# Optimization experiments

Measured on AMD Instinct MI355X. Metric: run time of the kernel, lower is better.

## Reference

```python
import jax, jax.numpy as jnp
import numpy as np

B, N, DN, DT = 1024, 200, 128, 128
M = DN + DN + DT  # model_dim = 384 (node + edge + time dims)


def setup_inputs() -> dict:
    key = jax.random.key(0)
    ks = jax.random.split(key, 10)
    rn = lambda k, s, sc=1.0: jax.random.normal(k, s, jnp.float32) * sc
    return {
        'src': rn(ks[0], (B, DN)),
        'src_t': rn(ks[1], (B, 1, DT)),
        'seq': rn(ks[2], (B, N, DN)),
        'seq_t': rn(ks[3], (B, N, DT)),
        'seq_e': rn(ks[4], (B, N, DN)),
        'mask': jax.random.randint(ks[5], (B, N), 0, 2).astype(bool),
        'shared_attn': rn(ks[6], (1, 2 * M), 0.05),
        'fc_w': rn(ks[7], (M, M), 0.05),
        'ln_g': jnp.ones((M,), jnp.float32),
        'ln_b': jnp.zeros((M,), jnp.float32),
        'agg_fc_w1': rn(ks[8], (2 * DN, M + DN), 0.05),
        'agg_fc_w2': rn(ks[9], (DN, 2 * DN), 0.05),
    }


def _layer_norm(x, g, b, eps=1e-5):
    mu = x.mean(-1, keepdims=True)
    var = ((x - mu) ** 2).mean(-1, keepdims=True)
    return (x - mu) * jax.lax.rsqrt(var + eps) * g + b


def reference(src, src_t, seq, seq_t, seq_e, mask, shared_attn, fc_w, ln_g, ln_b, agg_fc_w1, agg_fc_w2):
    # AttnModel.forward with 'simple' Attention (eval mode: dropout off)
    src_ext = src[:, None, :]                                   # [B,1,DN]
    q = jnp.concatenate([src_ext, jnp.zeros_like(src_ext), src_t], axis=2)  # [B,1,M]
    k = jnp.concatenate([seq, seq_e, seq_t], axis=2)            # [B,N,M]
    # F.linear(cat([q_exp, k_exp], -1), shared_attn) == q.w_q + k.w_k (fused, avoids [B,1,N,2M])
    w = shared_attn[0]
    wq, wk = w[:M], w[M:]
    scores = jnp.einsum('bqd,d->bq', q, wq)[:, :, None] + jnp.einsum('bnd,d->bn', k, wk)[:, None, :]  # [B,1,N]
    scores = jnp.where(mask[:, None, :], -1e10, scores)
    attn = jax.nn.softmax(scores, axis=2)                       # [B,1,N]
    out = jnp.einsum('bqn,bnm->bqm', attn, k)                   # [B,1,M] (v == k)
    out = out @ fc_w.T
    out = _layer_norm(out + q, ln_g, ln_b)
    out = out[:, 0, :]                                          # [B,M]
    attn_w = attn[:, 0, :]                                      # [B,N]
    x = jnp.concatenate([out, src], axis=1)                     # [B, M+DN]
    x = jax.nn.relu(x @ agg_fc_w1.T)                            # [B, 2*DN]
    out = x @ agg_fc_w2.T                                       # [B, DN]
    return out, attn_w
```

## Files before the change

kernel.cpp:

```cpp
#include <hip/hip_runtime.h>


constexpr int B_   = 1024;
constexpr int N_   = 200;
constexpr int DN_  = 128;
constexpr int DT_  = 128;
constexpr int M_   = 384;
constexpr int BDIM = 512;
constexpr int ROWS = 2;
constexpr int WPR  = 4;
constexpr int NPW  = N_ / WPR;
constexpr int PAIRS = NPW / 2;

__device__ float g_fcT[M_ * M_];
__device__ float g_w1T[(M_ + DN_) * (2 * DN_)];
__device__ float g_w2T[(2 * DN_) * DN_];

__device__ __forceinline__ float half_sum(float v) {
#pragma unroll
    for (int off = 16; off > 0; off >>= 1) v += __shfl_xor(v, off, 64);
    return v;
}
__device__ __forceinline__ float wave_sum(float v) {
#pragma unroll
    for (int off = 32; off > 0; off >>= 1) v += __shfl_xor(v, off, 64);
    return v;
}

__global__ void transpose_weights(const float* __restrict__ fc_w,
                                  const float* __restrict__ w1,
                                  const float* __restrict__ w2) {
    const int stride = gridDim.x * blockDim.x;
    for (int idx = blockIdx.x * blockDim.x + threadIdx.x; idx < M_ * M_; idx += stride) {
        const int j = idx / M_, i = idx - j * M_;
        g_fcT[idx] = fc_w[i * M_ + j];
    }
    for (int idx = blockIdx.x * blockDim.x + threadIdx.x; idx < (M_ + DN_) * (2 * DN_); idx += stride) {
        const int j = idx >> 8, i = idx & 255;
        g_w1T[idx] = w1[i * (M_ + DN_) + j];
    }
    for (int idx = blockIdx.x * blockDim.x + threadIdx.x; idx < (2 * DN_) * DN_; idx += stride) {
        const int j = idx >> 7, i = idx & 127;
        g_w2T[idx] = w2[i * (2 * DN_) + j];
    }
}

__global__ __launch_bounds__(BDIM)
void tgnn_kernel(
    const float* __restrict__ src,
    const float* __restrict__ src_t,
    const float* __restrict__ seq,
    const float* __restrict__ seq_t,
    const float* __restrict__ seq_e,
    const int*   __restrict__ mask,
    const float* __restrict__ shared_attn,
    const float* __restrict__ ln_g,
    const float* __restrict__ ln_b,
    float* __restrict__ out,
    float* __restrict__ attn_out)
{
    const int blk  = blockIdx.x;
    const int tid  = threadIdx.x;
    const int wave = tid >> 6;
    const int lane = tid & 63;
    const int row  = wave >> 2;
    const int wir  = wave & 3;
    const int b    = blk * ROWS + row;
    const int half = lane >> 5;
    const int sub  = lane & 31;
    const int c0   = 4 * sub;

    __shared__ float s_p[ROWS][N_];
    __shared__ float s_q[ROWS][M_];
    __shared__ float s_oa[8][M_];
    __shared__ float s_x[ROWS][M_];
    __shared__ float s_y[ROWS][M_ + DN_];
    __shared__ float s_h[ROWS][2 * DN_];
    __shared__ int   s_mask[ROWS][N_];
    __shared__ float s_red[ROWS][8];

    for (int idx = tid; idx < ROWS * M_; idx += BDIM) {
        const int r = idx / M_, d = idx - r * M_;
        const int bb = blk * ROWS + r;
        float v = (d < DN_) ? src[bb * DN_ + d]
                            : (d < 2 * DN_ ? 0.0f : src_t[bb * DT_ + (d - 2 * DN_)]);
        s_q[r][d] = v;
    }
    for (int idx = tid; idx < ROWS * N_; idx += BDIM) {
        const int r = idx / N_, n = idx - r * N_;
        s_mask[r][n] = mask[(blk * ROWS + r) * N_ + n];
    }

    const float* wq = shared_attn;
    const float* wk = shared_attn + M_;
    const float4 wkA = *(const float4*)&wk[c0];
    const float4 wkE = *(const float4*)&wk[DN_ + c0];
    const float4 wkT = *(const float4*)&wk[2 * DN_ + c0];
    const float4 wqA = *(const float4*)&wq[c0];
    const float4 wqT = *(const float4*)&wq[2 * DN_ + c0];

    __syncthreads();

    const float4 qa = *(const float4*)&s_q[row][c0];
    const float4 qt = *(const float4*)&s_q[row][2 * DN_ + c0];
    float qp = qa.x * wqA.x + qa.y * wqA.y + qa.z * wqA.z + qa.w * wqA.w
             + qt.x * wqT.x + qt.y * wqT.y + qt.z * wqT.z + qt.w * wqT.w;
    const float qdot = half_sum(qp);

    const int nb = wir * NPW + half;
    const float* baseA = seq   + (long)b * (N_ * DN_);
    const float* baseE = seq_e + (long)b * (N_ * DN_);
    const float* baseT = seq_t + (long)b * (N_ * DT_);
    int off = nb * DN_ + c0;
    int n   = nb;

    float4 oA = make_float4(0.f, 0.f, 0.f, 0.f);
    float4 oE = oA, oT = oA;
    float lsum = 0.f;

    int pairs = PAIRS;
    asm volatile("" : "+s"(pairs));
#pragma unroll 1
    for (int it = 0; it < pairs; ++it) {
        const float4 a = *(const float4*)(baseA + off);
        const float4 e = *(const float4*)(baseE + off);
        const float4 t = *(const float4*)(baseT + off);
        float part = a.x * wkA.x + a.y * wkA.y + a.z * wkA.z + a.w * wkA.w
                   + e.x * wkE.x + e.y * wkE.y + e.z * wkE.z + e.w * wkE.w
                   + t.x * wkT.x + t.y * wkT.y + t.z * wkT.z + t.w * wkT.w;
        part = half_sum(part);
        const float p = s_mask[row][n] ? 0.0f : __expf(part + qdot);
        if (sub == 0) s_p[row][n] = p;
        lsum += p;
        oA.x += p * a.x; oA.y += p * a.y; oA.z += p * a.z; oA.w += p * a.w;
        oE.x += p * e.x; oE.y += p * e.y; oE.z += p * e.z; oE.w += p * e.w;
        oT.x += p * t.x; oT.y += p * t.y; oT.z += p * t.z; oT.w += p * t.w;
        off += 2 * DN_;
        n   += 2;
    }

    oA.x += __shfl_xor(oA.x, 32, 64); oA.y += __shfl_xor(oA.y, 32, 64);
    oA.z += __shfl_xor(oA.z, 32, 64); oA.w += __shfl_xor(oA.w, 32, 64);
    oE.x += __shfl_xor(oE.x, 32, 64); oE.y += __shfl_xor(oE.y, 32, 64);
    oE.z += __shfl_xor(oE.z, 32, 64); oE.w += __shfl_xor(oE.w, 32, 64);
    oT.x += __shfl_xor(oT.x, 32, 64); oT.y += __shfl_xor(oT.y, 32, 64);
    oT.z += __shfl_xor(oT.z, 32, 64); oT.w += __shfl_xor(oT.w, 32, 64);
    lsum += __shfl_xor(lsum, 32, 64);
    if (lane == 0) s_red[row][wir] = lsum;
    if (half == 0) {
        *(float4*)&s_oa[wave][c0]            = oA;
        *(float4*)&s_oa[wave][DN_ + c0]      = oE;
        *(float4*)&s_oa[wave][2 * DN_ + c0]  = oT;
    }
    __syncthreads();

    for (int idx = tid; idx < ROWS * M_; idx += BDIM) {
        const int r = idx / M_, d = idx - r * M_;
        const float Z = s_red[r][0] + s_red[r][1] + s_red[r][2] + s_red[r][3];
        const float invZ = 1.0f / Z;
        s_x[r][d] = (s_oa[4 * r + 0][d] + s_oa[4 * r + 1][d] +
                     s_oa[4 * r + 2][d] + s_oa[4 * r + 3][d]) * invZ;
    }
    for (int idx = tid; idx < ROWS * N_; idx += BDIM) {
        const int r = idx / N_, nn = idx - r * N_;
        const float Z = s_red[r][0] + s_red[r][1] + s_red[r][2] + s_red[r][3];
        attn_out[(blk * ROWS + r) * N_ + nn] = s_p[r][nn] * (1.0f / Z);
    }
    __syncthreads();

    if (tid < M_) {
        float acc0 = 0.f, acc1 = 0.f;
#pragma unroll 8
        for (int j = 0; j < M_; ++j) {
            const float w = g_fcT[j * M_ + tid];
            acc0 += s_x[0][j] * w;
            acc1 += s_x[1][j] * w;
        }
        s_y[0][tid] = acc0 + s_q[0][tid];
        s_y[1][tid] = acc1 + s_q[1][tid];
    }
    __syncthreads();

    {
        float ls = 0.f, lq = 0.f;
        for (int j = 64 * wir + lane; j < M_; j += 256) {
            const float v = s_y[row][j];
            ls += v; lq += v * v;
        }
        ls = wave_sum(ls); lq = wave_sum(lq);
        if (lane == 0) { s_red[row][wir] = ls; s_red[row][4 + wir] = lq; }
    }
    __syncthreads();
    for (int idx = tid; idx < ROWS * M_; idx += BDIM) {
        const int r = idx / M_, j = idx - r * M_;
        const float mean = (s_red[r][0] + s_red[r][1] + s_red[r][2] + s_red[r][3]) * (1.0f / M_);
        const float msq  = (s_red[r][4] + s_red[r][5] + s_red[r][6] + s_red[r][7]) * (1.0f / M_);
        const float rstd = rsqrtf(msq - mean * mean + 1e-5f);
        s_y[r][j] = (s_y[r][j] - mean) * rstd * ln_g[j] + ln_b[j];
    }
    for (int idx = tid; idx < ROWS * DN_; idx += BDIM) {
        const int r = idx >> 7, d = idx & 127;
        s_y[r][M_ + d] = s_q[r][d];
    }
    __syncthreads();

    {
        const int r = tid >> 8, i = tid & 255;
        float acc = 0.f;
#pragma unroll 8
        for (int j = 0; j < M_ + DN_; ++j)
            acc += s_y[r][j] * g_w1T[j * 256 + i];
        s_h[r][i] = fmaxf(acc, 0.0f);
    }
    __syncthreads();

    if (tid < 256) {
        const int r = tid >> 7, i = tid & 127;
        float acc = 0.f;
#pragma unroll 8
        for (int j = 0; j < 2 * DN_; ++j)
            acc += s_h[r][j] * g_w2T[j * 128 + i];
        out[(blk * ROWS + r) * DN_ + i] = acc;
    }
}

extern "C" void kernel_launch(void* const* d_in, const int* in_sizes, int n_in,
                              void* d_out, int out_size, void* d_ws, size_t ws_size,
                              hipStream_t stream) {
    const float* src         = (const float*)d_in[0];
    const float* src_t       = (const float*)d_in[1];
    const float* seq         = (const float*)d_in[2];
    const float* seq_t       = (const float*)d_in[3];
    const float* seq_e       = (const float*)d_in[4];
    const int*   mask        = (const int*)  d_in[5];
    const float* shared_attn = (const float*)d_in[6];
    const float* fc_w        = (const float*)d_in[7];
    const float* ln_g        = (const float*)d_in[8];
    const float* ln_b        = (const float*)d_in[9];
    const float* w1          = (const float*)d_in[10];
    const float* w2          = (const float*)d_in[11];

    float* outp     = (float*)d_out;
    float* attn_out = (float*)d_out + B_ * DN_;

    transpose_weights<<<256, 256, 0, stream>>>(fc_w, w1, w2);
    tgnn_kernel<<<B_ / ROWS, BDIM, 0, stream>>>(src, src_t, seq, seq_t, seq_e, mask,
                                                shared_attn, ln_g, ln_b, outp, attn_out);
}
```

Measured before the change: 380.6 us.

## Double block size to 8 waves per row and split MLP reductions over K

```diff
diff --git a/kernel.cpp b/kernel.cpp
--- a/kernel.cpp
+++ b/kernel.cpp
@@ -6,11 +6,11 @@
 constexpr int DN_  = 128;
 constexpr int DT_  = 128;
 constexpr int M_   = 384;
-constexpr int BDIM = 512;
+constexpr int BDIM = 1024;
 constexpr int ROWS = 2;
-constexpr int WPR  = 4;
+constexpr int WPR  = 8;
 constexpr int NPW  = N_ / WPR;
-constexpr int PAIRS = NPW / 2;
+constexpr int ITER = (NPW + 1) / 2;
 
 __device__ float g_fcT[M_ * M_];
 __device__ float g_w1T[(M_ + DN_) * (2 * DN_)];
@@ -63,8 +63,8 @@
     const int tid  = threadIdx.x;
     const int wave = tid >> 6;
     const int lane = tid & 63;
-    const int row  = wave >> 2;
-    const int wir  = wave & 3;
+    const int row  = wave >> 3;
+    const int wir  = wave & 7;
     const int b    = blk * ROWS + row;
     const int half = lane >> 5;
     const int sub  = lane & 31;
@@ -72,12 +72,14 @@
 
     __shared__ float s_p[ROWS][N_];
     __shared__ float s_q[ROWS][M_];
-    __shared__ float s_oa[8][M_];
+    __shared__ float s_oa[16][M_];
     __shared__ float s_x[ROWS][M_];
     __shared__ float s_y[ROWS][M_ + DN_];
     __shared__ float s_h[ROWS][2 * DN_];
     __shared__ int   s_mask[ROWS][N_];
-    __shared__ float s_red[ROWS][8];
+    __shared__ float s_red[ROWS][16];
+    __shared__ float s_w1p[2][ROWS][256];
+    __shared__ float s_w2p[4][ROWS][128];
 
     for (int idx = tid; idx < ROWS * M_; idx += BDIM) {
         const int r = idx / M_, d = idx - r * M_;
@@ -107,21 +109,23 @@
              + qt.x * wqT.x + qt.y * wqT.y + qt.z * wqT.z + qt.w * wqT.w;
     const float qdot = half_sum(qp);
 
-    const int nb = wir * NPW + half;
+    const int kbase = wir * NPW;
     const float* baseA = seq   + (long)b * (N_ * DN_);
     const float* baseE = seq_e + (long)b * (N_ * DN_);
     const float* baseT = seq_t + (long)b * (N_ * DT_);
-    int off = nb * DN_ + c0;
-    int n   = nb;
 
     float4 oA = make_float4(0.f, 0.f, 0.f, 0.f);
     float4 oE = oA, oT = oA;
     float lsum = 0.f;
 
-    int pairs = PAIRS;
-    asm volatile("" : "+s"(pairs));
+    int iters = ITER;
+    asm volatile("" : "+s"(iters));
 #pragma unroll 1
-    for (int it = 0; it < pairs; ++it) {
+    for (int it = 0; it < iters; ++it) {
+        const int  ko    = 2 * it + half;
+        const bool valid = ko < NPW;
+        const int  n     = kbase + (valid ? ko : NPW - 1);
+        const int  off   = n * DN_ + c0;
         const float4 a = *(const float4*)(baseA + off);
         const float4 e = *(const float4*)(baseE + off);
         const float4 t = *(const float4*)(baseT + off);
@@ -129,14 +133,12 @@
                    + e.x * wkE.x + e.y * wkE.y + e.z * wkE.z + e.w * wkE.w
                    + t.x * wkT.x + t.y * wkT.y + t.z * wkT.z + t.w * wkT.w;
         part = half_sum(part);
-        const float p = s_mask[row][n] ? 0.0f : __expf(part + qdot);
-        if (sub == 0) s_p[row][n] = p;
+        const float p = (valid && !s_mask[row][n]) ? __expf(part + qdot) : 0.0f;
+        if (sub == 0 && valid) s_p[row][n] = p;
         lsum += p;
         oA.x += p * a.x; oA.y += p * a.y; oA.z += p * a.z; oA.w += p * a.w;
         oE.x += p * e.x; oE.y += p * e.y; oE.z += p * e.z; oE.w += p * e.w;
         oT.x += p * t.x; oT.y += p * t.y; oT.z += p * t.z; oT.w += p * t.w;
-        off += 2 * DN_;
-        n   += 2;
     }
 
     oA.x += __shfl_xor(oA.x, 32, 64); oA.y += __shfl_xor(oA.y, 32, 64);
@@ -156,15 +158,13 @@
 
     for (int idx = tid; idx < ROWS * M_; idx += BDIM) {
         const int r = idx / M_, d = idx - r * M_;
-        const float Z = s_red[r][0] + s_red[r][1] + s_red[r][2] + s_red[r][3];
+        const float Z = s_red[r][0] + s_red[r][1] + s_red[r][2] + s_red[r][3]
+                      + s_red[r][4] + s_red[r][5] + s_red[r][6] + s_red[r][7];
         const float invZ = 1.0f / Z;
-        s_x[r][d] = (s_oa[4 * r + 0][d] + s_oa[4 * r + 1][d] +
-                     s_oa[4 * r + 2][d] + s_oa[4 * r + 3][d]) * invZ;
-    }
-    for (int idx = tid; idx < ROWS * N_; idx += BDIM) {
-        const int r = idx / N_, nn = idx - r * N_;
-        const float Z = s_red[r][0] + s_red[r][1] + s_red[r][2] + s_red[r][3];
-        attn_out[(blk * ROWS + r) * N_ + nn] = s_p[r][nn] * (1.0f / Z);
+        float acc = 0.f;
+#pragma unroll
+        for (int w = 0; w < 8; ++w) acc += s_oa[8 * r + w][d];
+        s_x[r][d] = acc * invZ;
     }
     __syncthreads();
 
@@ -178,23 +178,34 @@
         }
         s_y[0][tid] = acc0 + s_q[0][tid];
         s_y[1][tid] = acc1 + s_q[1][tid];
+    } else if (tid < M_ + 256) {
+        const int t2 = tid - M_;
+        for (int idx = t2; idx < ROWS * N_; idx += 256) {
+            const int r = idx / N_, nn = idx - r * N_;
+            const float Z = s_red[r][0] + s_red[r][1] + s_red[r][2] + s_red[r][3]
+                          + s_red[r][4] + s_red[r][5] + s_red[r][6] + s_red[r][7];
+            attn_out[(blk * ROWS + r) * N_ + nn] = s_p[r][nn] * (1.0f / Z);
+        }
     }
     __syncthreads();
 
     {
         float ls = 0.f, lq = 0.f;
-        for (int j = 64 * wir + lane; j < M_; j += 256) {
+        for (int j = 64 * wir + lane; j < M_; j += 512) {
             const float v = s_y[row][j];
             ls += v; lq += v * v;
         }
         ls = wave_sum(ls); lq = wave_sum(lq);
-        if (lane == 0) { s_red[row][wir] = ls; s_red[row][4 + wir] = lq; }
+        if (lane == 0) { s_red[row][wir] = ls; s_red[row][8 + wir] = lq; }
     }
     __syncthreads();
     for (int idx = tid; idx < ROWS * M_; idx += BDIM) {
         const int r = idx / M_, j = idx - r * M_;
-        const float mean = (s_red[r][0] + s_red[r][1] + s_red[r][2] + s_red[r][3]) * (1.0f / M_);
-        const float msq  = (s_red[r][4] + s_red[r][5] + s_red[r][6] + s_red[r][7]) * (1.0f / M_);
+        float sm = 0.f, sq2 = 0.f;
+#pragma unroll
+        for (int w = 0; w < 8; ++w) { sm += s_red[r][w]; sq2 += s_red[r][8 + w]; }
+        const float mean = sm * (1.0f / M_);
+        const float msq  = sq2 * (1.0f / M_);
         const float rstd = rsqrtf(msq - mean * mean + 1e-5f);
         s_y[r][j] = (s_y[r][j] - mean) * rstd * ln_g[j] + ln_b[j];
     }
@@ -204,23 +215,44 @@
     }
     __syncthreads();
 
-    {
+    if (tid < 512) {
+        const int kk = tid >> 8, i = tid & 255;
+        const int j0 = kk * 256;
+        float acc0 = 0.f, acc1 = 0.f;
+#pragma unroll 8
+        for (int j = j0; j < j0 + 256; ++j) {
+            const float w = g_w1T[j * 256 + i];
+            acc0 += s_y[0][j] * w;
+            acc1 += s_y[1][j] * w;
+        }
+        s_w1p[kk][0][i] = acc0;
+        s_w1p[kk][1][i] = acc1;
+    }
+    __syncthreads();
+    if (tid < 512) {
         const int r = tid >> 8, i = tid & 255;
-        float acc = 0.f;
+        s_h[r][i] = fmaxf(s_w1p[0][r][i] + s_w1p[1][r][i], 0.0f);
+    }
+    __syncthreads();
+
+    if (tid < 512) {
+        const int kk = tid >> 7, i = tid & 127;
+        const int j0 = kk * 64;
+        float acc0 = 0.f, acc1 = 0.f;
 #pragma unroll 8
-        for (int j = 0; j < M_ + DN_; ++j)
-            acc += s_y[r][j] * g_w1T[j * 256 + i];
-        s_h[r][i] = fmaxf(acc, 0.0f);
-    }
-    __syncthreads();
-
+        for (int j = j0; j < j0 + 64; ++j) {
+            const float w = g_w2T[j * 128 + i];
+            acc0 += s_h[0][j] * w;
+            acc1 += s_h[1][j] * w;
+        }
+        s_w2p[kk][0][i] = acc0;
+        s_w2p[kk][1][i] = acc1;
+    }
+    __syncthreads();
     if (tid < 256) {
         const int r = tid >> 7, i = tid & 127;
-        float acc = 0.f;
-#pragma unroll 8
-        for (int j = 0; j < 2 * DN_; ++j)
-            acc += s_h[r][j] * g_w2T[j * 128 + i];
-        out[(blk * ROWS + r) * DN_ + i] = acc;
+        out[(blk * ROWS + r) * DN_ + i] =
+            s_w2p[0][r][i] + s_w2p[1][r][i] + s_w2p[2][r][i] + s_w2p[3][r][i];
     }
 }
 
```

After: 356.5 us. 6.3% less time.
